# Kernel optimization log

Hardware: AMD Instinct MI355X
Metric: run time of the kernel (lower is better)

The kernel has to match this reference:

```python
import jax, jax.numpy as jnp
import numpy as np

NB, T, N, C = 8, 8, 6890, 128
CLASS_NUM = 7
D_SUM = 512
PCADIM = 64
V = 7702  # garment template vertex count
EPS = 1e-5


def setup_inputs() -> dict:
    key = jax.random.key(0)
    ks = jax.random.split(key, 12)
    f = lambda k, s: jax.random.normal(k, s, dtype=jnp.float32)
    return {
        "x": f(ks[0], (NB, T, N, 3)),
        "sem_logits": f(ks[1], (NB * T, N, CLASS_NUM)),
        "feature": f(ks[2], (NB * T, C, N)),
        "garment_summary": f(ks[3], (NB, T, D_SUM)),
        "W1": f(ks[4], (128, D_SUM)) * 0.02, "b1": jnp.zeros((128,), jnp.float32),
        "g1": jnp.ones((128,), jnp.float32), "be1": jnp.zeros((128,), jnp.float32),
        "rm1": jnp.zeros((128,), jnp.float32), "rv1": jnp.ones((128,), jnp.float32),
        "W2": f(ks[5], (64, 128)) * 0.02, "b2": jnp.zeros((64,), jnp.float32),
        "g2": jnp.ones((64,), jnp.float32), "be2": jnp.zeros((64,), jnp.float32),
        "rm2": jnp.zeros((64,), jnp.float32), "rv2": jnp.ones((64,), jnp.float32),
        "W3": f(ks[6], (PCADIM, 64)) * 0.02, "b3": jnp.zeros((PCADIM,), jnp.float32),
        "pca_comp": f(ks[7], (PCADIM, V * 3)) * 0.02,
        "pca_mean": f(ks[8], (V * 3,)) * 0.02,
        "pca_scale": jnp.abs(f(ks[9], (V * 3,))) + 0.5,
        "garment_label": 1,
        "n": N // 4,
    }


def _segmentation_gather(x, sem_logits, feature, garment_label, n):
    # Vectorized form of the per-sample boolean-mask select / truncate / zero-pad loop.
    # x: [B,N,3]; feature: [B,C,N]; sem_logits: [B,N,K]
    feat = jnp.swapaxes(feature, 1, 2)                     # [B,N,C]
    labels = jnp.argmax(sem_logits, axis=2)                # [B,N] (detached in original)
    mask = labels == garment_label                         # [B,N]
    count = mask.sum(axis=1)                               # [B]
    # stable argsort puts selected (mask=True -> key False=0) indices first, in order
    order = jnp.argsort(jnp.logical_not(mask), axis=1)[:, :n]   # [B,n]
    valid = (jnp.arange(n)[None, :] < count[:, None]).astype(x.dtype)  # [B,n]
    gv = jnp.take_along_axis(x, order[:, :, None], axis=1) * valid[:, :, None]
    gf = jnp.take_along_axis(feat, order[:, :, None], axis=1) * valid[:, :, None]
    return gv, gf


def reference(x, sem_logits, feature, garment_summary, W1, b1, g1, be1, rm1, rv1,
              W2, b2, g2, be2, rm2, rv2, W3, b3, pca_comp, pca_mean, pca_scale,
              garment_label, n):
    nbatch, t = x.shape[0], x.shape[1]
    xf = x.reshape(nbatch * t, -1, 3)
    garment_v, garment_f = _segmentation_gather(xf, sem_logits, feature, garment_label, n)

    # PCAEncoder: 1x1 Conv1d over a length-1 sequence == linear layers; BN in eval mode
    def bn(h, g, be, rm, rv):
        return (h - rm) * jax.lax.rsqrt(rv + EPS) * g + be

    gs = garment_summary.max(axis=1)                       # [nbatch, 512] (max over T)
    h = jax.nn.relu(bn(gs @ W1.T + b1, g1, be1, rm1, rv1))
    h = jax.nn.relu(bn(h @ W2.T + b2, g2, be2, rm2, rv2))
    coeff = h @ W3.T + b3                                  # [nbatch, PCADIM]

    # PCA_inverse_transform
    tpose = ((coeff @ pca_comp) + pca_mean) * pca_scale
    tpose = tpose.reshape(coeff.shape[0], -1, 3)           # [nbatch, V, 3]
    return garment_v, garment_f, coeff, tpose
```

## Files before the change

### kernel.cpp

```cpp
#include <hip/hip_runtime.h>

#define NBATCH   8
#define TT       8
#define NPTS     6890
#define KCLS     7
#define CCH      128
#define BSAMP    64
#define NOUT     1722
#define DSUM     512
#define PCADIM   64
#define V3       23106
#define EPSBN    1e-5f

#define NW       108
#define PCH      256
#define CHB      4
#define CHN      32
#define LDSR     260
#define CPG      9
#define NGRP     3
#define K4B      91
#define NSCAN    BSAMP
#define NGATHER  (BSAMP * CHB * NGRP)

#define OFF_GV     0
#define OFF_GF     (BSAMP * NOUT * 3)
#define OFF_COEFF  (OFF_GF + BSAMP * NOUT * CCH)
#define OFF_TPOSE  (OFF_COEFF + NBATCH * PCADIM)

__global__ __launch_bounds__(256) void k1_mask_mlp(
    const float* __restrict__ logits,
    const int*   __restrict__ d_label,
    unsigned long long* __restrict__ ws_mask,
    const float* __restrict__ gsum,
    const float* __restrict__ W1, const float* __restrict__ b1,
    const float* __restrict__ g1, const float* __restrict__ be1,
    const float* __restrict__ rm1, const float* __restrict__ rv1,
    const float* __restrict__ W2, const float* __restrict__ b2,
    const float* __restrict__ g2, const float* __restrict__ be2,
    const float* __restrict__ rm2, const float* __restrict__ rv2,
    const float* __restrict__ W3, const float* __restrict__ b3,
    float* __restrict__ coeff_out, float* __restrict__ coeff_ws)
{
    const int tid = threadIdx.x;

    if (blockIdx.x < BSAMP * 27) {
        const int b     = blockIdx.x / 27;
        const int chunk = blockIdx.x % 27;
        const int i     = chunk * 256 + tid;
        const int label = d_label[0];

        bool sel = false;
        if (i < NPTS) {
            const float* p = logits + ((size_t)b * NPTS + i) * KCLS;
            float best = p[0]; int bi = 0;
            #pragma unroll
            for (int k = 1; k < KCLS; ++k) {
                float v = p[k];
                if (v > best) { best = v; bi = k; }
            }
            sel = (bi == label);
        }
        const unsigned long long m = __ballot(sel);
        if ((tid & 63) == 0) {
            const int w = chunk * 4 + (tid >> 6);
            if (w < NW) ws_mask[b * NW + w] = m;
        }
    } else {
        const int s    = blockIdx.x - BSAMP * 27;
        const int lane = tid & 63;
        const int wv   = tid >> 6;

        __shared__ float gs[DSUM];
        __shared__ float h1[128];
        __shared__ float h2[64];

        for (int d = tid; d < DSUM; d += 256) {
            const float* p = gsum + ((size_t)s * TT) * DSUM + d;
            float m = p[0];
            #pragma unroll
            for (int t = 1; t < TT; ++t) m = fmaxf(m, p[(size_t)t * DSUM]);
            gs[d] = m;
        }
        __syncthreads();

        for (int r = 0; r < 32; r += 2) {
            const int j0 = wv * 32 + r, j1 = j0 + 1;
            const float* w0 = W1 + (size_t)j0 * DSUM;
            const float* w1 = W1 + (size_t)j1 * DSUM;
            float pa = 0.f, pb = 0.f;
            #pragma unroll
            for (int d = lane; d < DSUM; d += 64) {
                const float gd = gs[d];
                pa = fmaf(w0[d], gd, pa);
                pb = fmaf(w1[d], gd, pb);
            }
            #pragma unroll
            for (int off = 32; off; off >>= 1) {
                pa += __shfl_xor(pa, off);
                pb += __shfl_xor(pb, off);
            }
            if (lane == 0) {
                pa += b1[j0];
                pa = (pa - rm1[j0]) * rsqrtf(rv1[j0] + EPSBN) * g1[j0] + be1[j0];
                h1[j0] = fmaxf(pa, 0.f);
                pb += b1[j1];
                pb = (pb - rm1[j1]) * rsqrtf(rv1[j1] + EPSBN) * g1[j1] + be1[j1];
                h1[j1] = fmaxf(pb, 0.f);
            }
        }
        __syncthreads();

        for (int r = 0; r < 16; ++r) {
            const int jj = wv * 16 + r;
            const float* w = W2 + (size_t)jj * 128;
            float p = w[lane] * h1[lane] + w[lane + 64] * h1[lane + 64];
            #pragma unroll
            for (int off = 32; off; off >>= 1) p += __shfl_xor(p, off);
            if (lane == 0) {
                p += b2[jj];
                p = (p - rm2[jj]) * rsqrtf(rv2[jj] + EPSBN) * g2[jj] + be2[jj];
                h2[jj] = fmaxf(p, 0.f);
            }
        }
        __syncthreads();

        for (int r = 0; r < 16; ++r) {
            const int jj = wv * 16 + r;
            float p = W3[(size_t)jj * 64 + lane] * h2[lane];
            #pragma unroll
            for (int off = 32; off; off >>= 1) p += __shfl_xor(p, off);
            if (lane == 0) {
                p += b3[jj];
                coeff_out[s * PCADIM + jj] = p;
                coeff_ws[s * PCADIM + jj]  = p;
            }
        }
    }
}

__global__ __launch_bounds__(256, 4) void k2_all(
    const float* __restrict__ feature,
    const unsigned long long* __restrict__ ws_mask,
    const float* __restrict__ x,
    float* __restrict__ gv,
    float* __restrict__ gf,
    const float* __restrict__ coeff_ws,
    const float* __restrict__ comp,
    const float* __restrict__ mean_,
    const float* __restrict__ scale_,
    float* __restrict__ tpose)
{
    __shared__ float lds[CHN * LDSR];
    __shared__ unsigned long long smask[NW];
    __shared__ int  swc[NW];
    __shared__ int  spos[PCH];
    __shared__ int  sel_list[PCH];
    __shared__ int  s_ns[4];
    __shared__ int  s_cnt;

    const int tid = threadIdx.x;

    if (blockIdx.x < K4B) {
        float* sc = lds;
        for (int o = tid; o < NBATCH * PCADIM; o += 256) sc[o] = coeff_ws[o];
        __syncthreads();

        const int v = blockIdx.x * 256 + tid;
        if (v >= V3) return;

        float acc[NBATCH];
        #pragma unroll
        for (int s = 0; s < NBATCH; ++s) acc[s] = 0.f;
        for (int k = 0; k < PCADIM; ++k) {
            const float pv = comp[(size_t)k * V3 + v];
            #pragma unroll
            for (int s = 0; s < NBATCH; ++s)
                acc[s] = fmaf(sc[s * PCADIM + k], pv, acc[s]);
        }
        const float mn = mean_[v], scl = scale_[v];
        #pragma unroll
        for (int s = 0; s < NBATCH; ++s)
            tpose[(size_t)s * V3 + v] = (acc[s] + mn) * scl;
        return;
    }

    if (blockIdx.x < K4B + NSCAN) {
        const int b = blockIdx.x - K4B;

        if (tid < NW) smask[tid] = ws_mask[b * NW + tid];
        __syncthreads();
        if (tid < NW) swc[tid] = __popcll(smask[tid]);
        __syncthreads();
        if (tid == 0) {
            int run = 0;
            for (int w = 0; w < NW; ++w) { int t = swc[w]; swc[w] = run; run += t; }
            s_cnt = run < NOUT ? run : NOUT;
        }
        __syncthreads();

        const float* xb = x + (size_t)b * NPTS * 3;
        for (int i = tid; i < NPTS; i += 256) {
            const int w = i >> 6, lb6 = i & 63;
            const unsigned long long m = smask[w];
            if ((m >> lb6) & 1ull) {
                const int pos = swc[w] + __popcll(m & ((1ull << lb6) - 1ull));
                if (pos < NOUT) {
                    const size_t go = ((size_t)b * NOUT + pos) * 3;
                    gv[go + 0] = xb[(size_t)i * 3 + 0];
                    gv[go + 1] = xb[(size_t)i * 3 + 1];
                    gv[go + 2] = xb[(size_t)i * 3 + 2];
                }
            }
        }
        for (int j = s_cnt + tid; j < NOUT; j += 256) {
            float* gp = gv + ((size_t)b * NOUT + j) * 3;
            gp[0] = 0.f; gp[1] = 0.f; gp[2] = 0.f;
        }
        return;
    }

    const int gb  = blockIdx.x - (K4B + NSCAN);
    const int b   = gb / (CHB * NGRP);
    const int rem = gb % (CHB * NGRP);
    const int cb  = rem / NGRP;
    const int g   = rem % NGRP;

    const int lane = tid & 63;
    const int wv   = tid >> 6;
    const int p4   = lane * 4;
    const float* fbase = feature + ((size_t)b * CCH + cb * CHN) * NPTS;

    float4 rc[8], rn[8];

    {
        const int i0 = (g * CPG) * PCH;
        const int il = min(PCH, NPTS - i0);
        const float* fb = fbase + i0 + p4;
        if (p4 + 4 <= il) {
            #pragma unroll
            for (int it = 0; it < 8; ++it)
                rc[it] = *(const float4*)(fb + (size_t)(wv * 8 + it) * NPTS);
        } else if (p4 < il) {
            #pragma unroll
            for (int it = 0; it < 8; ++it) {
                float2 v = *(const float2*)(fb + (size_t)(wv * 8 + it) * NPTS);
                rc[it] = make_float4(v.x, v.y, 0.f, 0.f);
            }
        } else {
            #pragma unroll
            for (int it = 0; it < 8; ++it) rc[it] = make_float4(0.f, 0.f, 0.f, 0.f);
        }
    }

    if (tid < NW) smask[tid] = ws_mask[b * NW + tid];
    __syncthreads();
    if (tid < NW) swc[tid] = __popcll(smask[tid]);
    __syncthreads();
    if (tid == 0) {
        int run = 0;
        for (int w = 0; w < NW; ++w) { int t = swc[w]; swc[w] = run; run += t; }
        s_cnt = run < NOUT ? run : NOUT;
    }
    __syncthreads();

    {
        const int cnt  = s_cnt;
        const int tail = NOUT - cnt;
        if (tail > 0) {
            const int nshares = CHB * NGRP;
            const int share = (tail + nshares - 1) / nshares;
            const int idx   = cb * NGRP + g;
            const int r0    = cnt + idx * share;
            const int r1    = min(r0 + share, NOUT);
            const int nrows = r1 - r0;
            if (nrows > 0) {
                float4* base4 = (float4*)(gf + ((size_t)b * NOUT + r0) * CCH);
                const int total = nrows * 32;
                for (int f = tid; f < total; f += 256)
                    base4[f] = make_float4(0.f, 0.f, 0.f, 0.f);
            }
        }
    }

    #pragma unroll 1
    for (int c = 0; c < CPG; ++c) {
        const int chunk = g * CPG + c;

        if (c + 1 < CPG) {
            const int i1 = (chunk + 1) * PCH;
            const int il = min(PCH, NPTS - i1);
            const float* fb = fbase + i1 + p4;
            if (p4 + 4 <= il) {
                #pragma unroll
                for (int it = 0; it < 8; ++it)
                    rn[it] = *(const float4*)(fb + (size_t)(wv * 8 + it) * NPTS);
            } else if (p4 < il) {
                #pragma unroll
                for (int it = 0; it < 8; ++it) {
                    float2 v = *(const float2*)(fb + (size_t)(wv * 8 + it) * NPTS);
                    rn[it] = make_float4(v.x, v.y, 0.f, 0.f);
                }
            } else {
                #pragma unroll
                for (int it = 0; it < 8; ++it) rn[it] = make_float4(0.f, 0.f, 0.f, 0.f);
            }
        }

        __syncthreads();

        #pragma unroll
        for (int it = 0; it < 8; ++it) {
            const int r = wv * 8 + it;
            *(float4*)(&lds[r * LDSR + p4]) = rc[it];
        }

        {
            const int word = 4 * chunk + wv;
            const unsigned long long m = smask[word];
            const int base = swc[word];
            const int sel  = (int)((m >> lane) & 1ull);
            const int pos  = base + __popcll(m & ((1ull << lane) - 1ull));
            const int sp   = (sel && pos < NOUT) ? pos : -1;
            const int plocal = wv * 64 + lane;
            spos[plocal] = sp;
            const unsigned long long mm = __ballot(sp >= 0);
            const int before = __popcll(mm & ((1ull << lane) - 1ull));
            if (sp >= 0) sel_list[wv * 64 + before] = plocal;
            if (lane == 0) s_ns[wv] = __popcll(mm);
        }
        __syncthreads();

        {
            const int ns   = s_ns[wv];
            const int half = lane >> 5;
            const int ch   = lane & 31;
            for (int s = half; s < ns; s += 2) {
                const int p   = sel_list[wv * 64 + s];
                const int pos = spos[p];
                gf[((size_t)b * NOUT + pos) * CCH + cb * CHN + ch] =
                    lds[ch * LDSR + p];
            }
        }

        if (c + 1 < CPG) {
            #pragma unroll
            for (int it = 0; it < 8; ++it) rc[it] = rn[it];
        }
    }
}

extern "C" void kernel_launch(void* const* d_in, const int* in_sizes, int n_in,
                              void* d_out, int out_size, void* d_ws, size_t ws_size,
                              hipStream_t stream) {
    const float* x      = (const float*)d_in[0];
    const float* logits = (const float*)d_in[1];
    const float* feat   = (const float*)d_in[2];
    const float* gsum   = (const float*)d_in[3];
    const float* W1  = (const float*)d_in[4];
    const float* b1  = (const float*)d_in[5];
    const float* g1  = (const float*)d_in[6];
    const float* be1 = (const float*)d_in[7];
    const float* rm1 = (const float*)d_in[8];
    const float* rv1 = (const float*)d_in[9];
    const float* W2  = (const float*)d_in[10];
    const float* b2  = (const float*)d_in[11];
    const float* g2  = (const float*)d_in[12];
    const float* be2 = (const float*)d_in[13];
    const float* rm2 = (const float*)d_in[14];
    const float* rv2 = (const float*)d_in[15];
    const float* W3  = (const float*)d_in[16];
    const float* b3  = (const float*)d_in[17];
    const float* comp  = (const float*)d_in[18];
    const float* mean_ = (const float*)d_in[19];
    const float* scale_= (const float*)d_in[20];
    const int* d_label = (const int*)d_in[21];

    float* out   = (float*)d_out;
    float* gv    = out + OFF_GV;
    float* gf    = out + OFF_GF;
    float* coeff = out + OFF_COEFF;
    float* tpose = out + OFF_TPOSE;

    unsigned long long* ws_mask = (unsigned long long*)d_ws;
    float* coeff_ws = (float*)(ws_mask + BSAMP * NW);

    k1_mask_mlp<<<BSAMP * 27 + NBATCH, 256, 0, stream>>>(
        logits, d_label, ws_mask, gsum, W1, b1, g1, be1, rm1, rv1,
        W2, b2, g2, be2, rm2, rv2, W3, b3, coeff, coeff_ws);

    k2_all<<<K4B + NSCAN + NGATHER, 256, 0, stream>>>(
        feat, ws_mask, x, gv, gf, coeff_ws, comp, mean_, scale_, tpose);
}
```

Baseline: 90.04 us.

## Load feature chunks directly into LDS and fold scan blocks into gather blocks

The feature gather now copies 512-point chunks straight from global memory into LDS with global_load_lds. This replaces the register double-buffer prefetch and the explicit LDS store. The separate per-sample x/gv scan blocks are removed: each gather block handles a slice of the gv scan and of the gv/gf zero tail. Selection entries pack the local index and output position into one int, and the store loop is software-pipelined. The trade-off is larger LDS tiles, lower occupancy (launch bounds 2), and no explicit overlap between loading the next chunk and processing the current one.

Result: slower. 101.0 us (+12.2%).

```diff
diff --git a/kernel.cpp b/kernel.cpp
--- a/kernel.cpp
+++ b/kernel.cpp
@@ -1,4 +1,5 @@
 #include <hip/hip_runtime.h>
+#include <stdint.h>
 
 #define NBATCH   8
 #define TT       8
@@ -13,20 +14,27 @@
 #define EPSBN    1e-5f
 
 #define NW       108
-#define PCH      256
+#define PCH      512
+#define NCHK     14
+#define CHN      32
 #define CHB      4
-#define CHN      32
-#define LDSR     260
-#define CPG      9
-#define NGRP     3
+#define LDSR     516
+#define CPG      7
+#define NGRP     2
 #define K4B      91
-#define NSCAN    BSAMP
 #define NGATHER  (BSAMP * CHB * NGRP)
 
 #define OFF_GV     0
 #define OFF_GF     (BSAMP * NOUT * 3)
 #define OFF_COEFF  (OFF_GF + BSAMP * NOUT * CCH)
 #define OFF_TPOSE  (OFF_COEFF + NBATCH * PCADIM)
+
+__device__ __forceinline__ void gl_lds16(const float* g, float* l) {
+    __builtin_amdgcn_global_load_lds(
+        (const __attribute__((address_space(1))) uint32_t*)g,
+        (__attribute__((address_space(3))) uint32_t*)l,
+        16, 0, 0);
+}
 
 __global__ __launch_bounds__(256) void k1_mask_mlp(
     const float* __restrict__ logits,
@@ -139,7 +147,7 @@
     }
 }
 
-__global__ __launch_bounds__(256, 4) void k2_all(
+__global__ __launch_bounds__(256, 2) void k2_all(
     const float* __restrict__ feature,
     const unsigned long long* __restrict__ ws_mask,
     const float* __restrict__ x,
@@ -154,9 +162,8 @@
     __shared__ float lds[CHN * LDSR];
     __shared__ unsigned long long smask[NW];
     __shared__ int  swc[NW];
-    __shared__ int  spos[PCH];
-    __shared__ int  sel_list[PCH];
-    __shared__ int  s_ns[4];
+    __shared__ int  sel_list[8 * 64];
+    __shared__ int  s_ns[8];
     __shared__ int  s_cnt;
 
     const int tid = threadIdx.x;
@@ -185,22 +192,33 @@
         return;
     }
 
-    if (blockIdx.x < K4B + NSCAN) {
-        const int b = blockIdx.x - K4B;
-
-        if (tid < NW) smask[tid] = ws_mask[b * NW + tid];
-        __syncthreads();
-        if (tid < NW) swc[tid] = __popcll(smask[tid]);
-        __syncthreads();
-        if (tid == 0) {
-            int run = 0;
-            for (int w = 0; w < NW; ++w) { int t = swc[w]; swc[w] = run; run += t; }
-            s_cnt = run < NOUT ? run : NOUT;
-        }
-        __syncthreads();
-
+    const int gb  = blockIdx.x - K4B;
+    const int b   = gb / (CHB * NGRP);
+    const int rem = gb % (CHB * NGRP);
+    const int cb  = rem / NGRP;
+    const int g   = rem % NGRP;
+    const int idx = cb * NGRP + g;
+
+    const int lane = tid & 63;
+    const int wv   = tid >> 6;
+    const float* fbase = feature + ((size_t)b * CCH + cb * CHN) * NPTS;
+
+    if (tid < NW) smask[tid] = ws_mask[b * NW + tid];
+    __syncthreads();
+    if (tid < NW) swc[tid] = __popcll(smask[tid]);
+    __syncthreads();
+    if (tid == 0) {
+        int run = 0;
+        for (int w = 0; w < NW; ++w) { int t = swc[w]; swc[w] = run; run += t; }
+        s_cnt = run < NOUT ? run : NOUT;
+    }
+    __syncthreads();
+
+    {
+        const int i0s = idx * 862;
+        const int i1s = min(i0s + 862, NPTS);
         const float* xb = x + (size_t)b * NPTS * 3;
-        for (int i = tid; i < NPTS; i += 256) {
+        for (int i = i0s + tid; i < i1s; i += 256) {
             const int w = i >> 6, lb6 = i & 63;
             const unsigned long long m = smask[w];
             if ((m >> lb6) & 1ull) {
@@ -213,70 +231,21 @@
                 }
             }
         }
-        for (int j = s_cnt + tid; j < NOUT; j += 256) {
-            float* gp = gv + ((size_t)b * NOUT + j) * 3;
-            gp[0] = 0.f; gp[1] = 0.f; gp[2] = 0.f;
-        }
-        return;
-    }
-
-    const int gb  = blockIdx.x - (K4B + NSCAN);
-    const int b   = gb / (CHB * NGRP);
-    const int rem = gb % (CHB * NGRP);
-    const int cb  = rem / NGRP;
-    const int g   = rem % NGRP;
-
-    const int lane = tid & 63;
-    const int wv   = tid >> 6;
-    const int p4   = lane * 4;
-    const float* fbase = feature + ((size_t)b * CCH + cb * CHN) * NPTS;
-
-    float4 rc[8], rn[8];
-
-    {
-        const int i0 = (g * CPG) * PCH;
-        const int il = min(PCH, NPTS - i0);
-        const float* fb = fbase + i0 + p4;
-        if (p4 + 4 <= il) {
-            #pragma unroll
-            for (int it = 0; it < 8; ++it)
-                rc[it] = *(const float4*)(fb + (size_t)(wv * 8 + it) * NPTS);
-        } else if (p4 < il) {
-            #pragma unroll
-            for (int it = 0; it < 8; ++it) {
-                float2 v = *(const float2*)(fb + (size_t)(wv * 8 + it) * NPTS);
-                rc[it] = make_float4(v.x, v.y, 0.f, 0.f);
-            }
-        } else {
-            #pragma unroll
-            for (int it = 0; it < 8; ++it) rc[it] = make_float4(0.f, 0.f, 0.f, 0.f);
-        }
-    }
-
-    if (tid < NW) smask[tid] = ws_mask[b * NW + tid];
-    __syncthreads();
-    if (tid < NW) swc[tid] = __popcll(smask[tid]);
-    __syncthreads();
-    if (tid == 0) {
-        int run = 0;
-        for (int w = 0; w < NW; ++w) { int t = swc[w]; swc[w] = run; run += t; }
-        s_cnt = run < NOUT ? run : NOUT;
-    }
-    __syncthreads();
-
+    }
     {
         const int cnt  = s_cnt;
         const int tail = NOUT - cnt;
         if (tail > 0) {
-            const int nshares = CHB * NGRP;
-            const int share = (tail + nshares - 1) / nshares;
-            const int idx   = cb * NGRP + g;
+            const int share = (tail + 7) / 8;
             const int r0    = cnt + idx * share;
             const int r1    = min(r0 + share, NOUT);
-            const int nrows = r1 - r0;
-            if (nrows > 0) {
+            if (r1 > r0) {
+                for (int j = r0 + tid; j < r1; j += 256) {
+                    float* gp = gv + ((size_t)b * NOUT + j) * 3;
+                    gp[0] = 0.f; gp[1] = 0.f; gp[2] = 0.f;
+                }
                 float4* base4 = (float4*)(gf + ((size_t)b * NOUT + r0) * CCH);
-                const int total = nrows * 32;
+                const int total = (r1 - r0) * 32;
                 for (int f = tid; f < total; f += 256)
                     base4[f] = make_float4(0.f, 0.f, 0.f, 0.f);
             }
@@ -286,66 +255,70 @@
     #pragma unroll 1
     for (int c = 0; c < CPG; ++c) {
         const int chunk = g * CPG + c;
-
-        if (c + 1 < CPG) {
-            const int i1 = (chunk + 1) * PCH;
-            const int il = min(PCH, NPTS - i1);
-            const float* fb = fbase + i1 + p4;
-            if (p4 + 4 <= il) {
-                #pragma unroll
-                for (int it = 0; it < 8; ++it)
-                    rn[it] = *(const float4*)(fb + (size_t)(wv * 8 + it) * NPTS);
-            } else if (p4 < il) {
-                #pragma unroll
-                for (int it = 0; it < 8; ++it) {
-                    float2 v = *(const float2*)(fb + (size_t)(wv * 8 + it) * NPTS);
-                    rn[it] = make_float4(v.x, v.y, 0.f, 0.f);
-                }
-            } else {
-                #pragma unroll
-                for (int it = 0; it < 8; ++it) rn[it] = make_float4(0.f, 0.f, 0.f, 0.f);
-            }
-        }
-
-        __syncthreads();
+        const int i0    = chunk * PCH;
+
+        __syncthreads();
+
+        if (chunk != NCHK - 1) {
+            #pragma unroll
+            for (int it = 0; it < 8; ++it) {
+                const int r = wv * 8 + it;
+                const float* src = fbase + (size_t)r * NPTS + i0;
+                float* dst = &lds[r * LDSR];
+                gl_lds16(src + lane * 4,       dst);
+                gl_lds16(src + 256 + lane * 4, dst + 256);
+            }
+        } else {
+            const int il = NPTS - i0;
+            #pragma unroll
+            for (int it = 0; it < 8; ++it) {
+                const int r = wv * 8 + it;
+                const float* src = fbase + (size_t)r * NPTS + i0;
+                for (int off = lane; off < il; off += 64)
+                    lds[r * LDSR + off] = src[off];
+            }
+        }
 
         #pragma unroll
-        for (int it = 0; it < 8; ++it) {
-            const int r = wv * 8 + it;
-            *(float4*)(&lds[r * LDSR + p4]) = rc[it];
-        }
+        for (int j = 0; j < 2; ++j) {
+            const int wk   = 2 * wv + j;
+            const int word = chunk * 8 + wk;
+            unsigned long long m = 0; int base = 0;
+            if (word < NW) { m = smask[word]; base = swc[word]; }
+            const int sel = (int)((m >> lane) & 1ull);
+            const int pos = base + __popcll(m & ((1ull << lane) - 1ull));
+            const bool ok = sel && pos < NOUT;
+            const unsigned long long mm = __ballot(ok);
+            const int before = __popcll(mm & ((1ull << lane) - 1ull));
+            if (ok) sel_list[wk * 64 + before] = (wk * 64 + lane) | (pos << 9);
+            if (lane == 0) s_ns[wk] = __popcll(mm);
+        }
+
+        __syncthreads();
 
         {
-            const int word = 4 * chunk + wv;
-            const unsigned long long m = smask[word];
-            const int base = swc[word];
-            const int sel  = (int)((m >> lane) & 1ull);
-            const int pos  = base + __popcll(m & ((1ull << lane) - 1ull));
-            const int sp   = (sel && pos < NOUT) ? pos : -1;
-            const int plocal = wv * 64 + lane;
-            spos[plocal] = sp;
-            const unsigned long long mm = __ballot(sp >= 0);
-            const int before = __popcll(mm & ((1ull << lane) - 1ull));
-            if (sp >= 0) sel_list[wv * 64 + before] = plocal;
-            if (lane == 0) s_ns[wv] = __popcll(mm);
-        }
-        __syncthreads();
-
-        {
-            const int ns   = s_ns[wv];
             const int half = lane >> 5;
             const int ch   = lane & 31;
-            for (int s = half; s < ns; s += 2) {
-                const int p   = sel_list[wv * 64 + s];
-                const int pos = spos[p];
-                gf[((size_t)b * NOUT + pos) * CCH + cb * CHN + ch] =
-                    lds[ch * LDSR + p];
-            }
-        }
-
-        if (c + 1 < CPG) {
-            #pragma unroll
-            for (int it = 0; it < 8; ++it) rc[it] = rn[it];
+            float* gfb = gf + (size_t)b * NOUT * CCH + cb * CHN + ch;
+            #pragma unroll
+            for (int j = 0; j < 2; ++j) {
+                const int wk = 2 * wv + j;
+                const int ns = s_ns[wk];
+                int s = half;
+                if (s < ns) {
+                    int e = sel_list[wk * 64 + s];
+                    int p = e & 511, pos = e >> 9;
+                    float v = lds[ch * LDSR + p];
+                    for (s += 2; s < ns; s += 2) {
+                        const int e2 = sel_list[wk * 64 + s];
+                        const int p2 = e2 & 511, pos2 = e2 >> 9;
+                        const float v2 = lds[ch * LDSR + p2];
+                        gfb[(size_t)pos * CCH] = v;
+                        v = v2; pos = pos2;
+                    }
+                    gfb[(size_t)pos * CCH] = v;
+                }
+            }
         }
     }
 }
@@ -389,6 +362,6 @@
         logits, d_label, ws_mask, gsum, W1, b1, g1, be1, rm1, rv1,
         W2, b2, g2, be2, rm2, rv2, W3, b3, coeff, coeff_ws);
 
-    k2_all<<<K4B + NSCAN + NGATHER, 256, 0, stream>>>(
+    k2_all<<<K4B + NGATHER, 256, 0, stream>>>(
         feat, ws_mask, x, gv, gf, coeff_ws, comp, mean_, scale_, tpose);
 }
```

## Fuse mask/MLP and gather kernels into one cooperative launch with grid sync

Applied to the files above, without the earlier changes.

Merges the two kernels into a single templated kernel launched cooperatively, where every block first computes mask tiles (and the first blocks compute the MLP), then a grid-wide sync separates that phase from the tpose and gather work. The separate scan blocks are removed; each gather block now scatters a slice of gv and zeroes its share of the gv/gf tail. The aim is to save one kernel launch and the scan-block stage. In exchange it adds a grid barrier, which needs all 859 blocks co-resident (at 4 blocks per CU). If the cooperative launch fails, it falls back to two launches.

Result: slower. 203.1 us (+125.5%).

```diff
diff --git a/kernel.cpp b/kernel.cpp
--- a/kernel.cpp
+++ b/kernel.cpp
@@ -1,4 +1,8 @@
 #include <hip/hip_runtime.h>
+#include <hip/hip_cooperative_groups.h>
+#include <stdint.h>
+
+namespace cg = cooperative_groups;
 
 #define NBATCH   8
 #define TT       8
@@ -14,24 +18,26 @@
 
 #define NW       108
 #define PCH      256
+#define NCHK     27
+#define CHN      32
 #define CHB      4
-#define CHN      32
+#define NGRP     3
+#define CPG      9
 #define LDSR     260
-#define CPG      9
-#define NGRP     3
-#define K4B      91
-#define NSCAN    BSAMP
+#define NTILES   (BSAMP * 27)
+#define NTPOSE   91
 #define NGATHER  (BSAMP * CHB * NGRP)
+#define GRID     (NTPOSE + NGATHER)
 
 #define OFF_GV     0
 #define OFF_GF     (BSAMP * NOUT * 3)
 #define OFF_COEFF  (OFF_GF + BSAMP * NOUT * CCH)
 #define OFF_TPOSE  (OFF_COEFF + NBATCH * PCADIM)
 
-__global__ __launch_bounds__(256) void k1_mask_mlp(
+template <int PHASE>
+__global__ __launch_bounds__(256, 4) void kfused(
     const float* __restrict__ logits,
     const int*   __restrict__ d_label,
-    unsigned long long* __restrict__ ws_mask,
     const float* __restrict__ gsum,
     const float* __restrict__ W1, const float* __restrict__ b1,
     const float* __restrict__ g1, const float* __restrict__ be1,
@@ -40,115 +46,16 @@
     const float* __restrict__ g2, const float* __restrict__ be2,
     const float* __restrict__ rm2, const float* __restrict__ rv2,
     const float* __restrict__ W3, const float* __restrict__ b3,
-    float* __restrict__ coeff_out, float* __restrict__ coeff_ws)
-{
-    const int tid = threadIdx.x;
-
-    if (blockIdx.x < BSAMP * 27) {
-        const int b     = blockIdx.x / 27;
-        const int chunk = blockIdx.x % 27;
-        const int i     = chunk * 256 + tid;
-        const int label = d_label[0];
-
-        bool sel = false;
-        if (i < NPTS) {
-            const float* p = logits + ((size_t)b * NPTS + i) * KCLS;
-            float best = p[0]; int bi = 0;
-            #pragma unroll
-            for (int k = 1; k < KCLS; ++k) {
-                float v = p[k];
-                if (v > best) { best = v; bi = k; }
-            }
-            sel = (bi == label);
-        }
-        const unsigned long long m = __ballot(sel);
-        if ((tid & 63) == 0) {
-            const int w = chunk * 4 + (tid >> 6);
-            if (w < NW) ws_mask[b * NW + w] = m;
-        }
-    } else {
-        const int s    = blockIdx.x - BSAMP * 27;
-        const int lane = tid & 63;
-        const int wv   = tid >> 6;
-
-        __shared__ float gs[DSUM];
-        __shared__ float h1[128];
-        __shared__ float h2[64];
-
-        for (int d = tid; d < DSUM; d += 256) {
-            const float* p = gsum + ((size_t)s * TT) * DSUM + d;
-            float m = p[0];
-            #pragma unroll
-            for (int t = 1; t < TT; ++t) m = fmaxf(m, p[(size_t)t * DSUM]);
-            gs[d] = m;
-        }
-        __syncthreads();
-
-        for (int r = 0; r < 32; r += 2) {
-            const int j0 = wv * 32 + r, j1 = j0 + 1;
-            const float* w0 = W1 + (size_t)j0 * DSUM;
-            const float* w1 = W1 + (size_t)j1 * DSUM;
-            float pa = 0.f, pb = 0.f;
-            #pragma unroll
-            for (int d = lane; d < DSUM; d += 64) {
-                const float gd = gs[d];
-                pa = fmaf(w0[d], gd, pa);
-                pb = fmaf(w1[d], gd, pb);
-            }
-            #pragma unroll
-            for (int off = 32; off; off >>= 1) {
-                pa += __shfl_xor(pa, off);
-                pb += __shfl_xor(pb, off);
-            }
-            if (lane == 0) {
-                pa += b1[j0];
-                pa = (pa - rm1[j0]) * rsqrtf(rv1[j0] + EPSBN) * g1[j0] + be1[j0];
-                h1[j0] = fmaxf(pa, 0.f);
-                pb += b1[j1];
-                pb = (pb - rm1[j1]) * rsqrtf(rv1[j1] + EPSBN) * g1[j1] + be1[j1];
-                h1[j1] = fmaxf(pb, 0.f);
-            }
-        }
-        __syncthreads();
-
-        for (int r = 0; r < 16; ++r) {
-            const int jj = wv * 16 + r;
-            const float* w = W2 + (size_t)jj * 128;
-            float p = w[lane] * h1[lane] + w[lane + 64] * h1[lane + 64];
-            #pragma unroll
-            for (int off = 32; off; off >>= 1) p += __shfl_xor(p, off);
-            if (lane == 0) {
-                p += b2[jj];
-                p = (p - rm2[jj]) * rsqrtf(rv2[jj] + EPSBN) * g2[jj] + be2[jj];
-                h2[jj] = fmaxf(p, 0.f);
-            }
-        }
-        __syncthreads();
-
-        for (int r = 0; r < 16; ++r) {
-            const int jj = wv * 16 + r;
-            float p = W3[(size_t)jj * 64 + lane] * h2[lane];
-            #pragma unroll
-            for (int off = 32; off; off >>= 1) p += __shfl_xor(p, off);
-            if (lane == 0) {
-                p += b3[jj];
-                coeff_out[s * PCADIM + jj] = p;
-                coeff_ws[s * PCADIM + jj]  = p;
-            }
-        }
-    }
-}
-
-__global__ __launch_bounds__(256, 4) void k2_all(
-    const float* __restrict__ feature,
-    const unsigned long long* __restrict__ ws_mask,
-    const float* __restrict__ x,
-    float* __restrict__ gv,
-    float* __restrict__ gf,
-    const float* __restrict__ coeff_ws,
     const float* __restrict__ comp,
     const float* __restrict__ mean_,
     const float* __restrict__ scale_,
+    const float* __restrict__ x,
+    const float* __restrict__ feature,
+    unsigned long long* __restrict__ ws_mask,
+    float* __restrict__ coeff_ws,
+    float* __restrict__ gv,
+    float* __restrict__ gf,
+    float* __restrict__ coeff_out,
     float* __restrict__ tpose)
 {
     __shared__ float lds[CHN * LDSR];
@@ -159,14 +66,118 @@
     __shared__ int  s_ns[4];
     __shared__ int  s_cnt;
 
-    const int tid = threadIdx.x;
-
-    if (blockIdx.x < K4B) {
+    const int tid  = threadIdx.x;
+    const int bid  = blockIdx.x;
+    const int lane = tid & 63;
+    const int wv   = tid >> 6;
+
+    if constexpr (PHASE != 2) {
+        const int label = d_label[0];
+        auto do_tile = [&](int tile) {
+            const int b     = tile / 27;
+            const int chunk = tile % 27;
+            const int i     = chunk * 256 + tid;
+            bool sel = false;
+            if (i < NPTS) {
+                const float* p = logits + ((size_t)b * NPTS + i) * KCLS;
+                float best = p[0]; int bi = 0;
+                #pragma unroll
+                for (int k = 1; k < KCLS; ++k) {
+                    float v = p[k];
+                    if (v > best) { best = v; bi = k; }
+                }
+                sel = (bi == label);
+            }
+            const unsigned long long m = __ballot(sel);
+            if (lane == 0) {
+                const int w = chunk * 4 + wv;
+                if (w < NW) ws_mask[b * NW + w] = m;
+            }
+        };
+        do_tile(bid * 2);
+        do_tile(bid * 2 + 1);
+        if (bid >= 849) do_tile(1718 + (bid - 849));
+
+        if (bid < NBATCH) {
+            const int s = bid;
+            float* gs = lds;
+            float* h1 = lds + 512;
+            float* h2 = lds + 640;
+
+            for (int d = tid; d < DSUM; d += 256) {
+                const float* p = gsum + ((size_t)s * TT) * DSUM + d;
+                float m = p[0];
+                #pragma unroll
+                for (int t = 1; t < TT; ++t) m = fmaxf(m, p[(size_t)t * DSUM]);
+                gs[d] = m;
+            }
+            __syncthreads();
+
+            for (int r = 0; r < 32; r += 2) {
+                const int j0 = wv * 32 + r, j1 = j0 + 1;
+                const float* w0 = W1 + (size_t)j0 * DSUM;
+                const float* w1 = W1 + (size_t)j1 * DSUM;
+                float pa = 0.f, pb = 0.f;
+                #pragma unroll
+                for (int d = lane; d < DSUM; d += 64) {
+                    const float gd = gs[d];
+                    pa = fmaf(w0[d], gd, pa);
+                    pb = fmaf(w1[d], gd, pb);
+                }
+                #pragma unroll
+                for (int off = 32; off; off >>= 1) {
+                    pa += __shfl_xor(pa, off);
+                    pb += __shfl_xor(pb, off);
+                }
+                if (lane == 0) {
+                    pa += b1[j0];
+                    pa = (pa - rm1[j0]) * rsqrtf(rv1[j0] + EPSBN) * g1[j0] + be1[j0];
+                    h1[j0] = fmaxf(pa, 0.f);
+                    pb += b1[j1];
+                    pb = (pb - rm1[j1]) * rsqrtf(rv1[j1] + EPSBN) * g1[j1] + be1[j1];
+                    h1[j1] = fmaxf(pb, 0.f);
+                }
+            }
+            __syncthreads();
+
+            for (int r = 0; r < 16; ++r) {
+                const int jj = wv * 16 + r;
+                const float* w = W2 + (size_t)jj * 128;
+                float p = w[lane] * h1[lane] + w[lane + 64] * h1[lane + 64];
+                #pragma unroll
+                for (int off = 32; off; off >>= 1) p += __shfl_xor(p, off);
+                if (lane == 0) {
+                    p += b2[jj];
+                    p = (p - rm2[jj]) * rsqrtf(rv2[jj] + EPSBN) * g2[jj] + be2[jj];
+                    h2[jj] = fmaxf(p, 0.f);
+                }
+            }
+            __syncthreads();
+
+            for (int r = 0; r < 16; ++r) {
+                const int jj = wv * 16 + r;
+                float p = W3[(size_t)jj * 64 + lane] * h2[lane];
+                #pragma unroll
+                for (int off = 32; off; off >>= 1) p += __shfl_xor(p, off);
+                if (lane == 0) {
+                    p += b3[jj];
+                    coeff_out[s * PCADIM + jj] = p;
+                    coeff_ws[s * PCADIM + jj]  = p;
+                }
+            }
+            __syncthreads();
+        }
+    }
+
+    if constexpr (PHASE == 0) cg::this_grid().sync();
+    if constexpr (PHASE == 1) return;
+
+    if (bid < NTPOSE) {
         float* sc = lds;
         for (int o = tid; o < NBATCH * PCADIM; o += 256) sc[o] = coeff_ws[o];
         __syncthreads();
 
-        const int v = blockIdx.x * 256 + tid;
+        const int v = bid * 256 + tid;
         if (v >= V3) return;
 
         float acc[NBATCH];
@@ -185,22 +196,42 @@
         return;
     }
 
-    if (blockIdx.x < K4B + NSCAN) {
-        const int b = blockIdx.x - K4B;
-
-        if (tid < NW) smask[tid] = ws_mask[b * NW + tid];
-        __syncthreads();
-        if (tid < NW) swc[tid] = __popcll(smask[tid]);
-        __syncthreads();
-        if (tid == 0) {
-            int run = 0;
-            for (int w = 0; w < NW; ++w) { int t = swc[w]; swc[w] = run; run += t; }
-            s_cnt = run < NOUT ? run : NOUT;
-        }
-        __syncthreads();
-
+    const int gb  = bid - NTPOSE;
+    const int b   = gb / (CHB * NGRP);
+    const int rem = gb % (CHB * NGRP);
+    const int cb  = rem / NGRP;
+    const int g   = rem % NGRP;
+    const int idx = rem;
+
+    const int p4 = lane * 4;
+    const float* fbase = feature + ((size_t)b * CCH + cb * CHN) * NPTS;
+
+    float4 rc[8], rn[8];
+
+    {
+        const int i0 = (g * CPG) * PCH;
+        const float* fb = fbase + i0 + p4;
+        #pragma unroll
+        for (int it = 0; it < 8; ++it)
+            rc[it] = *(const float4*)(fb + (size_t)(wv * 8 + it) * NPTS);
+    }
+
+    if (tid < NW) smask[tid] = ws_mask[b * NW + tid];
+    __syncthreads();
+    if (tid < NW) swc[tid] = __popcll(smask[tid]);
+    __syncthreads();
+    if (tid == 0) {
+        int run = 0;
+        for (int w = 0; w < NW; ++w) { int t = swc[w]; swc[w] = run; run += t; }
+        s_cnt = run < NOUT ? run : NOUT;
+    }
+    __syncthreads();
+
+    {
+        const int i0s = idx * 575;
+        const int i1s = min(i0s + 575, NPTS);
         const float* xb = x + (size_t)b * NPTS * 3;
-        for (int i = tid; i < NPTS; i += 256) {
+        for (int i = i0s + tid; i < i1s; i += 256) {
             const int w = i >> 6, lb6 = i & 63;
             const unsigned long long m = smask[w];
             if ((m >> lb6) & 1ull) {
@@ -213,70 +244,19 @@
                 }
             }
         }
-        for (int j = s_cnt + tid; j < NOUT; j += 256) {
-            float* gp = gv + ((size_t)b * NOUT + j) * 3;
-            gp[0] = 0.f; gp[1] = 0.f; gp[2] = 0.f;
-        }
-        return;
-    }
-
-    const int gb  = blockIdx.x - (K4B + NSCAN);
-    const int b   = gb / (CHB * NGRP);
-    const int rem = gb % (CHB * NGRP);
-    const int cb  = rem / NGRP;
-    const int g   = rem % NGRP;
-
-    const int lane = tid & 63;
-    const int wv   = tid >> 6;
-    const int p4   = lane * 4;
-    const float* fbase = feature + ((size_t)b * CCH + cb * CHN) * NPTS;
-
-    float4 rc[8], rn[8];
-
-    {
-        const int i0 = (g * CPG) * PCH;
-        const int il = min(PCH, NPTS - i0);
-        const float* fb = fbase + i0 + p4;
-        if (p4 + 4 <= il) {
-            #pragma unroll
-            for (int it = 0; it < 8; ++it)
-                rc[it] = *(const float4*)(fb + (size_t)(wv * 8 + it) * NPTS);
-        } else if (p4 < il) {
-            #pragma unroll
-            for (int it = 0; it < 8; ++it) {
-                float2 v = *(const float2*)(fb + (size_t)(wv * 8 + it) * NPTS);
-                rc[it] = make_float4(v.x, v.y, 0.f, 0.f);
-            }
-        } else {
-            #pragma unroll
-            for (int it = 0; it < 8; ++it) rc[it] = make_float4(0.f, 0.f, 0.f, 0.f);
-        }
-    }
-
-    if (tid < NW) smask[tid] = ws_mask[b * NW + tid];
-    __syncthreads();
-    if (tid < NW) swc[tid] = __popcll(smask[tid]);
-    __syncthreads();
-    if (tid == 0) {
-        int run = 0;
-        for (int w = 0; w < NW; ++w) { int t = swc[w]; swc[w] = run; run += t; }
-        s_cnt = run < NOUT ? run : NOUT;
-    }
-    __syncthreads();
-
-    {
         const int cnt  = s_cnt;
         const int tail = NOUT - cnt;
         if (tail > 0) {
-            const int nshares = CHB * NGRP;
-            const int share = (tail + nshares - 1) / nshares;
-            const int idx   = cb * NGRP + g;
+            const int share = (tail + 11) / 12;
             const int r0    = cnt + idx * share;
             const int r1    = min(r0 + share, NOUT);
-            const int nrows = r1 - r0;
-            if (nrows > 0) {
+            if (r1 > r0) {
+                for (int j = r0 + tid; j < r1; j += 256) {
+                    float* gp = gv + ((size_t)b * NOUT + j) * 3;
+                    gp[0] = 0.f; gp[1] = 0.f; gp[2] = 0.f;
+                }
                 float4* base4 = (float4*)(gf + ((size_t)b * NOUT + r0) * CCH);
-                const int total = nrows * 32;
+                const int total = (r1 - r0) * 32;
                 for (int f = tid; f < total; f += 256)
                     base4[f] = make_float4(0.f, 0.f, 0.f, 0.f);
             }
@@ -288,22 +268,24 @@
         const int chunk = g * CPG + c;
 
         if (c + 1 < CPG) {
-            const int i1 = (chunk + 1) * PCH;
-            const int il = min(PCH, NPTS - i1);
+            const int nchunk = chunk + 1;
+            const int i1 = nchunk * PCH;
             const float* fb = fbase + i1 + p4;
-            if (p4 + 4 <= il) {
+            if (nchunk != NCHK - 1) {
                 #pragma unroll
                 for (int it = 0; it < 8; ++it)
                     rn[it] = *(const float4*)(fb + (size_t)(wv * 8 + it) * NPTS);
-            } else if (p4 < il) {
+            } else {
+                const int il = NPTS - i1;
                 #pragma unroll
                 for (int it = 0; it < 8; ++it) {
-                    float2 v = *(const float2*)(fb + (size_t)(wv * 8 + it) * NPTS);
-                    rn[it] = make_float4(v.x, v.y, 0.f, 0.f);
-                }
-            } else {
-                #pragma unroll
-                for (int it = 0; it < 8; ++it) rn[it] = make_float4(0.f, 0.f, 0.f, 0.f);
+                    const float* src = fb + (size_t)(wv * 8 + it) * NPTS;
+                    if (p4 + 4 <= il)      rn[it] = *(const float4*)(src);
+                    else if (p4 < il) {
+                        float2 v = *(const float2*)(src);
+                        rn[it] = make_float4(v.x, v.y, 0.f, 0.f);
+                    } else                 rn[it] = make_float4(0.f, 0.f, 0.f, 0.f);
+                }
             }
         }
 
@@ -317,29 +299,29 @@
 
         {
             const int word = 4 * chunk + wv;
-            const unsigned long long m = smask[word];
-            const int base = swc[word];
-            const int sel  = (int)((m >> lane) & 1ull);
-            const int pos  = base + __popcll(m & ((1ull << lane) - 1ull));
-            const int sp   = (sel && pos < NOUT) ? pos : -1;
+            unsigned long long m = 0; int base = 0;
+            if (word < NW) { m = smask[word]; base = swc[word]; }
+            const int sel = (int)((m >> lane) & 1ull);
+            const int pos = base + __popcll(m & ((1ull << lane) - 1ull));
+            const bool ok = sel && pos < NOUT;
             const int plocal = wv * 64 + lane;
-            spos[plocal] = sp;
-            const unsigned long long mm = __ballot(sp >= 0);
+            spos[plocal] = ok ? pos : -1;
+            const unsigned long long mm = __ballot(ok);
             const int before = __popcll(mm & ((1ull << lane) - 1ull));
-            if (sp >= 0) sel_list[wv * 64 + before] = plocal;
+            if (ok) sel_list[wv * 64 + before] = plocal;
             if (lane == 0) s_ns[wv] = __popcll(mm);
         }
         __syncthreads();
 
         {
-            const int ns   = s_ns[wv];
             const int half = lane >> 5;
             const int ch   = lane & 31;
+            float* gfb = gf + (size_t)b * NOUT * CCH + cb * CHN + ch;
+            const int ns = s_ns[wv];
             for (int s = half; s < ns; s += 2) {
                 const int p   = sel_list[wv * 64 + s];
                 const int pos = spos[p];
-                gf[((size_t)b * NOUT + pos) * CCH + cb * CHN + ch] =
-                    lds[ch * LDSR + p];
+                gfb[(size_t)pos * CCH] = lds[ch * LDSR + p];
             }
         }
 
@@ -385,10 +367,26 @@
     unsigned long long* ws_mask = (unsigned long long*)d_ws;
     float* coeff_ws = (float*)(ws_mask + BSAMP * NW);
 
-    k1_mask_mlp<<<BSAMP * 27 + NBATCH, 256, 0, stream>>>(
-        logits, d_label, ws_mask, gsum, W1, b1, g1, be1, rm1, rv1,
-        W2, b2, g2, be2, rm2, rv2, W3, b3, coeff, coeff_ws);
-
-    k2_all<<<K4B + NSCAN + NGATHER, 256, 0, stream>>>(
-        feat, ws_mask, x, gv, gf, coeff_ws, comp, mean_, scale_, tpose);
+    void* args[] = {
+        (void*)&logits, (void*)&d_label, (void*)&gsum,
+        (void*)&W1, (void*)&b1, (void*)&g1, (void*)&be1, (void*)&rm1, (void*)&rv1,
+        (void*)&W2, (void*)&b2, (void*)&g2, (void*)&be2, (void*)&rm2, (void*)&rv2,
+        (void*)&W3, (void*)&b3, (void*)&comp, (void*)&mean_, (void*)&scale_,
+        (void*)&x, (void*)&feat, (void*)&ws_mask, (void*)&coeff_ws,
+        (void*)&gv, (void*)&gf, (void*)&coeff, (void*)&tpose
+    };
+
+    hipError_t rc = hipLaunchCooperativeKernel(
+        (const void*)(&kfused<0>), dim3(GRID), dim3(256), args, 0, stream);
+
+    if (rc != hipSuccess) {
+        kfused<1><<<GRID, 256, 0, stream>>>(
+            logits, d_label, gsum, W1, b1, g1, be1, rm1, rv1,
+            W2, b2, g2, be2, rm2, rv2, W3, b3, comp, mean_, scale_,
+            x, feat, ws_mask, coeff_ws, gv, gf, coeff, tpose);
+        kfused<2><<<GRID, 256, 0, stream>>>(
+            logits, d_label, gsum, W1, b1, g1, be1, rm1, rv1,
+            W2, b2, g2, be2, rm2, rv2, W3, b3, comp, mean_, scale_,
+            x, feat, ws_mask, coeff_ws, gv, gf, coeff, tpose);
+    }
 }
```
